# Kernel optimization log

Measured on AMD Instinct MI355X. Metric: run time of the kernel, lower is better.

The kernel has to match this reference:

```python
import jax, jax.numpy as jnp
import numpy as np

N_NODES = 50000
N_EDGES = 800000
D_IN = 128
H1 = 128
H2 = 64
N_CLASSES = 4


def _sage_conv(x, src, dst, w_l, w_r, b, num_nodes):
    # PyG SAGEConv (aggr='mean'): out = lin_l(mean_{j->i} x_j) + lin_r(x_i)
    ones = jnp.ones((src.shape[0],), dtype=x.dtype)
    deg = jax.ops.segment_sum(ones, dst, num_segments=num_nodes)  # [N]
    agg = jax.ops.segment_sum(x[src], dst, num_segments=num_nodes)  # [N, d]
    agg = agg / jnp.maximum(deg, 1.0)[:, None]
    return agg @ w_l + b + x @ w_r


def setup_inputs() -> dict:
    key = jax.random.key(0)
    ks = jax.random.split(key, 12)
    x_content = jax.random.normal(ks[0], (N_NODES, D_IN), dtype=jnp.float32)
    edge_index = jax.random.randint(ks[1], (2, N_EDGES), 0, N_NODES, dtype=jnp.int32)
    edge_type = jax.random.randint(ks[2], (N_EDGES,), 0, 4, dtype=jnp.int32)
    s = 0.05
    params = {
        'w_l0': jax.random.normal(ks[3], (D_IN, H1), jnp.float32) * s,
        'w_r0': jax.random.normal(ks[4], (D_IN, H1), jnp.float32) * s,
        'b0': jnp.zeros((H1,), jnp.float32),
        'w_l1': jax.random.normal(ks[5], (H1, H1), jnp.float32) * s,
        'w_r1': jax.random.normal(ks[6], (H1, H1), jnp.float32) * s,
        'b1': jnp.zeros((H1,), jnp.float32),
        'w_l2': jax.random.normal(ks[7], (H1, H2), jnp.float32) * s,
        'w_r2': jax.random.normal(ks[8], (H1, H2), jnp.float32) * s,
        'b2': jnp.zeros((H2,), jnp.float32),
        'w_out': jax.random.normal(ks[9], (H2, N_CLASSES), jnp.float32) * s,
        'b_out': jnp.zeros((N_CLASSES,), jnp.float32),
    }
    return {'x_content': x_content, 'edge_index': edge_index, 'edge_type': edge_type, **params}


def reference(x_content, edge_index, edge_type,
              w_l0, w_r0, b0, w_l1, w_r1, b1, w_l2, w_r2, b2, w_out, b_out):
    # eval mode: dropout is identity
    src, dst = edge_index[0], edge_index[1]
    n = x_content.shape[0]
    x = x_content
    for (wl, wr, b) in ((w_l0, w_r0, b0), (w_l1, w_r1, b1), (w_l2, w_r2, b2)):
        x = _sage_conv(x, src, dst, wl, wr, b, n)
        x = jax.nn.relu(x)
    return x @ w_out + b_out
```

## Files before the change

kernel.cpp:

```cpp
#include <hip/hip_runtime.h>
#include <hip/hip_fp16.h>

#define D 128

constexpr int RSH = 14;
constexpr int RSZ = 1 << RSH;
constexpr int NRANGE = 4;
constexpr int CSH = 15;
constexpr int CSZ = 1 << CSH;

using short8 = __attribute__((ext_vector_type(8))) short;
using f32x4 = __attribute__((ext_vector_type(4))) float;

__device__ inline void splitf(float v, unsigned short& h, unsigned short& l) {
    unsigned b = __float_as_uint(v);
    h = (unsigned short)(b >> 16);
    float fh = __uint_as_float(b & 0xffff0000u);
    float r = v - fh;
    l = (unsigned short)(__float_as_uint(r) >> 16);
}

struct WSplitArgs {
    const float* src[6];
    unsigned short* dh[6];
    unsigned short* dl[6];
    int n[6];
};

__global__ __launch_bounds__(256) void split_w(WSplitArgs a) {
    int m = blockIdx.y;
    int N = a.n[m];
    int e = blockIdx.x * 256 + threadIdx.x;
    if (e >= 128 * N) return;
    int sh = (N == 128) ? 7 : 6;
    int k = e >> sh;
    int n = e & (N - 1);
    float v = a.src[m][e];
    unsigned short h, l;
    splitf(v, h, l);
    a.dh[m][n * 128 + k] = h;
    a.dl[m][n * 128 + k] = l;
}

__global__ __launch_bounds__(1024) void hist_gemm_x(
    const int* __restrict__ dst, unsigned* __restrict__ hist,
    unsigned short* __restrict__ rank, int n_edges, int nchunk, int nhist,
    const float* __restrict__ X,
    const unsigned short* __restrict__ W1h, const unsigned short* __restrict__ W1l,
    const unsigned short* __restrict__ W2h, const unsigned short* __restrict__ W2l,
    const float* __restrict__ bias, __half* __restrict__ P, float* __restrict__ Q, int M) {
    __shared__ __align__(16) char smem[2 * 16 * 65 * 16];

    const int b = blockIdx.x;
    const int tid = threadIdx.x;

    if (b < nhist) {
        unsigned* lh = (unsigned*)smem;
        int r = b & (NRANGE - 1), c = b >> 2;
        for (int i = tid; i < RSZ / 2; i += 1024) lh[i] = 0;
        __syncthreads();
        int e0 = c << CSH, e1 = min(n_edges, e0 + CSZ);
        for (int e = e0 + tid; e < e1; e += 1024) {
            int d = dst[e];
            if ((d >> RSH) == r) {
                int ii = d & (RSZ - 1);
                unsigned sh = (ii & 1) * 16;
                unsigned old = atomicAdd(&lh[ii >> 1], 1u << sh);
                rank[e] = (unsigned short)((old >> sh) & 0xffffu);
            }
        }
        __syncthreads();
        unsigned* gh = hist + (size_t)(r * nchunk + c) * (RSZ / 2);
        for (int i = tid; i < RSZ / 2; i += 1024) gh[i] = lh[i];
        return;
    }

    short8(*As)[16 * 65] = (short8(*)[16 * 65])smem;
    const int wave = tid >> 6;
    const int lane = tid & 63;
    const int l15 = lane & 15;
    const int q = lane >> 4;
    const int m0 = (b - nhist) * 64;

    {
        int row = tid >> 4, col16 = tid & 15;
        int gr = min(m0 + row, M - 1);
        const float4* xp = (const float4*)X + (size_t)gr * 32 + col16 * 2;
        float4 v0 = xp[0], v1 = xp[1];
        float fv[8] = {v0.x, v0.y, v0.z, v0.w, v1.x, v1.y, v1.z, v1.w};
        short8 h, l;
#pragma unroll
        for (int j = 0; j < 8; ++j) {
            unsigned short hh_, ll_;
            splitf(fv[j], hh_, ll_);
            h[j] = (short)hh_;
            l[j] = (short)ll_;
        }
        As[0][col16 * 65 + row] = h;
        As[1][col16 * 65 + row] = l;
    }
    __syncthreads();

    const int isQ = wave >> 3;
    const int colbase = (wave & 7) * 16;
    const unsigned short* Wh = isQ ? W2h : W1h;
    const unsigned short* Wl = isQ ? W2l : W1l;
    const float bv = isQ ? bias[colbase + l15] : 0.f;

    f32x4 acc[4] = {};

#pragma unroll 1
    for (int kt = 0; kt < 4; ++kt) {
        int c = colbase + l15;
        int woff = c * 128 + kt * 32 + q * 8;
        short8 Bh = *(const short8*)(Wh + woff);
        short8 Bl = *(const short8*)(Wl + woff);
#pragma unroll
        for (int mt = 0; mt < 4; ++mt) {
            int ai = (kt * 4 + q) * 65 + mt * 16 + l15;
            short8 Afh = As[0][ai];
            short8 Afl = As[1][ai];
            acc[mt] = __builtin_amdgcn_mfma_f32_16x16x32_bf16(Afh, Bh, acc[mt], 0, 0, 0);
            acc[mt] = __builtin_amdgcn_mfma_f32_16x16x32_bf16(Afh, Bl, acc[mt], 0, 0, 0);
            acc[mt] = __builtin_amdgcn_mfma_f32_16x16x32_bf16(Afl, Bh, acc[mt], 0, 0, 0);
        }
    }

    const int col = colbase + l15;
#pragma unroll
    for (int mt = 0; mt < 4; ++mt) {
        int orow = m0 + mt * 16 + q * 4;
#pragma unroll
        for (int r = 0; r < 4; ++r) {
            int rr = orow + r;
            if (rr < M) {
                if (isQ) Q[(size_t)rr * 128 + col] = acc[mt][r] + bv;
                else P[(size_t)rr * 128 + col] = __float2half(acc[mt][r]);
            }
        }
    }
}

__global__ __launch_bounds__(256) void deg_sum_partials(
    const unsigned short* __restrict__ hist16, int* __restrict__ deg,
    int* __restrict__ partials, int n_nodes, int nchunk) {
    __shared__ int sd[256];
    int b = blockIdx.x, t = threadIdx.x;
    int i = b * 256 + t;
    int s = 0;
    if (i < n_nodes) {
        int r = i >> RSH, ii = i & (RSZ - 1);
        const unsigned short* hp = hist16 + (size_t)r * nchunk * RSZ + ii;
        for (int c = 0; c < nchunk; ++c) s += hp[(size_t)c * RSZ];
        deg[i] = s;
    }
    sd[t] = s;
    __syncthreads();
    for (int st = 128; st > 0; st >>= 1) {
        if (t < st) sd[t] += sd[t + st];
        __syncthreads();
    }
    if (t == 0) partials[b] = sd[0];
}

__global__ __launch_bounds__(256) void scan_fill(
    const int* __restrict__ deg, const int* __restrict__ partials,
    const unsigned short* __restrict__ hist16, int* __restrict__ row_ptr,
    float* __restrict__ inv_deg, int* __restrict__ base,
    int n_nodes, int nchunk, int nblk) {
    __shared__ int sp[256];
    __shared__ int sd[256];
    int b = blockIdx.x, t = threadIdx.x;

    sp[t] = (t < b && t < nblk) ? partials[t] : 0;
    __syncthreads();
    for (int st = 128; st > 0; st >>= 1) {
        if (t < st) sp[t] += sp[t + st];
        __syncthreads();
    }
    int pbase = sp[0];

    int i = b * 256 + t;
    int v = (i < n_nodes) ? deg[i] : 0;
    sd[t] = v;
    __syncthreads();
    for (int d = 1; d < 256; d <<= 1) {
        int x = (t >= d) ? sd[t - d] : 0;
        __syncthreads();
        sd[t] += x;
        __syncthreads();
    }
    int excl = sd[t] - v + pbase;
    if (i < n_nodes) {
        row_ptr[i] = excl;
        int dv = v > 1 ? v : 1;
        inv_deg[i] = 1.0f / (float)dv;
        if (i == n_nodes - 1) row_ptr[n_nodes] = excl + v;
        int r = i >> RSH, ii = i & (RSZ - 1);
        int bacc = excl;
        for (int c = 0; c < nchunk; ++c) {
            size_t idx = (size_t)(r * nchunk + c) * RSZ + ii;
            base[idx] = bacc;
            bacc += hist16[idx];
        }
    }
}

__global__ __launch_bounds__(256) void fill_edges(
    const int* __restrict__ src, const int* __restrict__ dst,
    const unsigned short* __restrict__ rank, const int* __restrict__ base,
    int* __restrict__ csr, int n_edges, int nchunk) {
    int e = blockIdx.x * 256 + threadIdx.x;
    if (e >= n_edges) return;
    int d = dst[e];
    int c = e >> CSH;
    int r = d >> RSH;
    int slot = base[(size_t)(r * nchunk + c) * RSZ + (d & (RSZ - 1))] + rank[e];
    csr[slot] = src[e];
}

template <int BN, int NT>
__global__ __launch_bounds__(256) void gemm_lds(
    const unsigned short* __restrict__ Ah, const unsigned short* __restrict__ Al,
    const unsigned short* __restrict__ W1h, const unsigned short* __restrict__ W1l,
    const unsigned short* __restrict__ W2h, const unsigned short* __restrict__ W2l,
    const float* __restrict__ bias, __half* __restrict__ P, float* __restrict__ Q, int M) {
    __shared__ short8 As[2][16 * 65];

    const int tid = threadIdx.x;
    const int wave = tid >> 6;
    const int lane = tid & 63;
    const int l15 = lane & 15;
    const int q = lane >> 4;
    const int m0 = blockIdx.x * 64;

#pragma unroll
    for (int it = 0; it < 8; ++it) {
        int s = it * 256 + tid;
        int arr = s >> 10;
        int sp = s & 1023;
        int row = sp >> 4, col16 = sp & 15;
        int gr = min(m0 + row, M - 1);
        const unsigned short* src = (arr ? Al : Ah) + (size_t)gr * 128 + col16 * 8;
        As[arr][col16 * 65 + row] = *(const short8*)src;
    }
    __syncthreads();

    const int isQ = wave >> 1;
    const int colbase = (wave & 1) * (NT * 16);
    const unsigned short* Wh = isQ ? W2h : W1h;
    const unsigned short* Wl = isQ ? W2l : W1l;

    float bvs[NT];
#pragma unroll
    for (int nt = 0; nt < NT; ++nt) bvs[nt] = isQ ? bias[colbase + nt * 16 + l15] : 0.f;

    f32x4 acc[4][NT] = {};

#pragma unroll 1
    for (int kt = 0; kt < 4; ++kt) {
        short8 Bh[NT], Bl[NT];
#pragma unroll
        for (int nt = 0; nt < NT; ++nt) {
            int c = colbase + nt * 16 + l15;
            int off = c * 128 + kt * 32 + q * 8;
            Bh[nt] = *(const short8*)(Wh + off);
            Bl[nt] = *(const short8*)(Wl + off);
        }
#pragma unroll
        for (int mt = 0; mt < 4; ++mt) {
            int ai = (kt * 4 + q) * 65 + mt * 16 + l15;
            short8 Afh = As[0][ai];
            short8 Afl = As[1][ai];
#pragma unroll
            for (int nt = 0; nt < NT; ++nt) {
                acc[mt][nt] = __builtin_amdgcn_mfma_f32_16x16x32_bf16(Afh, Bh[nt], acc[mt][nt], 0, 0, 0);
                acc[mt][nt] = __builtin_amdgcn_mfma_f32_16x16x32_bf16(Afh, Bl[nt], acc[mt][nt], 0, 0, 0);
                acc[mt][nt] = __builtin_amdgcn_mfma_f32_16x16x32_bf16(Afl, Bh[nt], acc[mt][nt], 0, 0, 0);
            }
        }
    }

#pragma unroll
    for (int mt = 0; mt < 4; ++mt) {
        int orow = m0 + mt * 16 + q * 4;
#pragma unroll
        for (int nt = 0; nt < NT; ++nt) {
            int col = colbase + nt * 16 + l15;
#pragma unroll
            for (int r = 0; r < 4; ++r) {
                int rr = orow + r;
                if (rr < M) {
                    if (isQ) Q[(size_t)rr * BN + col] = acc[mt][nt][r] + bvs[nt];
                    else P[(size_t)rr * BN + col] = __float2half(acc[mt][nt][r]);
                }
            }
        }
    }
}

__global__ __launch_bounds__(256) void agg_fused128(
    const __half* __restrict__ P, const float* __restrict__ Q,
    const int* __restrict__ row_ptr, const int* __restrict__ csr,
    const float* __restrict__ inv_deg, unsigned short* __restrict__ Hh,
    unsigned short* __restrict__ Hl, int n_nodes) {
    int node = (blockIdx.x * blockDim.x + threadIdx.x) >> 6;
    int lane = threadIdx.x & 63;
    if (node >= n_nodes) return;
    int beg = row_ptr[node], end = row_ptr[node + 1];
    const int g = lane >> 4;
    const int l = lane & 15;
    float a[4][8] = {};
    int e = beg;
    bool have = (e + 16 <= end);
    int i0 = 0, i1 = 0, i2 = 0, i3 = 0;
    if (have) { i0 = csr[e + g]; i1 = csr[e + 4 + g]; i2 = csr[e + 8 + g]; i3 = csr[e + 12 + g]; }
    while (have) {
        int en = e + 16;
        bool hn = (en + 16 <= end);
        int n0 = 0, n1 = 0, n2 = 0, n3 = 0;
        if (hn) { n0 = csr[en + g]; n1 = csr[en + 4 + g]; n2 = csr[en + 8 + g]; n3 = csr[en + 12 + g]; }
        int ss[4] = {i0, i1, i2, i3};
#pragma unroll
        for (int j = 0; j < 4; ++j) {
            uint4 raw = *(const uint4*)(P + (size_t)ss[j] * 128 + l * 8);
            float2 f01 = __half22float2(*reinterpret_cast<__half2*>(&raw.x));
            float2 f23 = __half22float2(*reinterpret_cast<__half2*>(&raw.y));
            float2 f45 = __half22float2(*reinterpret_cast<__half2*>(&raw.z));
            float2 f67 = __half22float2(*reinterpret_cast<__half2*>(&raw.w));
            a[j][0] += f01.x; a[j][1] += f01.y; a[j][2] += f23.x; a[j][3] += f23.y;
            a[j][4] += f45.x; a[j][5] += f45.y; a[j][6] += f67.x; a[j][7] += f67.y;
        }
        e = en; i0 = n0; i1 = n1; i2 = n2; i3 = n3; have = hn;
    }
    if (e < end) {
        int p0 = e + g, p1 = e + 4 + g, p2 = e + 8 + g, p3 = e + 12 + g;
        int j0 = (p0 < end) ? csr[p0] : -1;
        int j1 = (p1 < end) ? csr[p1] : -1;
        int j2 = (p2 < end) ? csr[p2] : -1;
        int j3 = (p3 < end) ? csr[p3] : -1;
        int ss[4] = {j0, j1, j2, j3};
#pragma unroll
        for (int j = 0; j < 4; ++j) {
            if (ss[j] >= 0) {
                uint4 raw = *(const uint4*)(P + (size_t)ss[j] * 128 + l * 8);
                float2 f01 = __half22float2(*reinterpret_cast<__half2*>(&raw.x));
                float2 f23 = __half22float2(*reinterpret_cast<__half2*>(&raw.y));
                float2 f45 = __half22float2(*reinterpret_cast<__half2*>(&raw.z));
                float2 f67 = __half22float2(*reinterpret_cast<__half2*>(&raw.w));
                a[j][0] += f01.x; a[j][1] += f01.y; a[j][2] += f23.x; a[j][3] += f23.y;
                a[j][4] += f45.x; a[j][5] += f45.y; a[j][6] += f67.x; a[j][7] += f67.y;
            }
        }
    }
    float s[8];
#pragma unroll
    for (int k = 0; k < 8; ++k) {
        s[k] = (a[0][k] + a[1][k]) + (a[2][k] + a[3][k]);
        s[k] += __shfl_xor(s[k], 16);
        s[k] += __shfl_xor(s[k], 32);
    }
    if (lane < 16) {
        float w = inv_deg[node];
        const float4* Q4 = (const float4*)Q;
        float4 q0 = Q4[(size_t)node * 32 + 2 * l];
        float4 q1 = Q4[(size_t)node * 32 + 2 * l + 1];
        float h0 = fmaxf(fmaf(s[0], w, q0.x), 0.f);
        float h1 = fmaxf(fmaf(s[1], w, q0.y), 0.f);
        float h2 = fmaxf(fmaf(s[2], w, q0.z), 0.f);
        float h3 = fmaxf(fmaf(s[3], w, q0.w), 0.f);
        float h4 = fmaxf(fmaf(s[4], w, q1.x), 0.f);
        float h5 = fmaxf(fmaf(s[5], w, q1.y), 0.f);
        float h6 = fmaxf(fmaf(s[6], w, q1.z), 0.f);
        float h7 = fmaxf(fmaf(s[7], w, q1.w), 0.f);
        ushort4 hv0, lv0, hv1, lv1;
        splitf(h0, hv0.x, lv0.x);
        splitf(h1, hv0.y, lv0.y);
        splitf(h2, hv0.z, lv0.z);
        splitf(h3, hv0.w, lv0.w);
        splitf(h4, hv1.x, lv1.x);
        splitf(h5, hv1.y, lv1.y);
        splitf(h6, hv1.z, lv1.z);
        splitf(h7, hv1.w, lv1.w);
        ((ushort4*)Hh)[(size_t)node * 32 + 2 * l] = hv0;
        ((ushort4*)Hh)[(size_t)node * 32 + 2 * l + 1] = hv1;
        ((ushort4*)Hl)[(size_t)node * 32 + 2 * l] = lv0;
        ((ushort4*)Hl)[(size_t)node * 32 + 2 * l + 1] = lv1;
    }
}

__global__ __launch_bounds__(256) void agg64_head(
    const __half* __restrict__ P, const float* __restrict__ Q,
    const int* __restrict__ row_ptr, const int* __restrict__ csr,
    const float* __restrict__ inv_deg, const float* __restrict__ Wo,
    const float* __restrict__ bo, float* __restrict__ out, int n_nodes) {
    int node = (blockIdx.x * blockDim.x + threadIdx.x) >> 6;
    int lane = threadIdx.x & 63;
    if (node >= n_nodes) return;
    int beg = row_ptr[node], end = row_ptr[node + 1];
    const int g = lane >> 4;
    const int l = lane & 15;
    float a[4][4] = {};
    int e = beg;
    bool have = (e + 16 <= end);
    int i0 = 0, i1 = 0, i2 = 0, i3 = 0;
    if (have) { i0 = csr[e + g]; i1 = csr[e + 4 + g]; i2 = csr[e + 8 + g]; i3 = csr[e + 12 + g]; }
    while (have) {
        int en = e + 16;
        bool hn = (en + 16 <= end);
        int n0 = 0, n1 = 0, n2 = 0, n3 = 0;
        if (hn) { n0 = csr[en + g]; n1 = csr[en + 4 + g]; n2 = csr[en + 8 + g]; n3 = csr[en + 12 + g]; }
        int ss[4] = {i0, i1, i2, i3};
#pragma unroll
        for (int j = 0; j < 4; ++j) {
            uint2 raw = *(const uint2*)(P + (size_t)ss[j] * 64 + l * 4);
            float2 f01 = __half22float2(*reinterpret_cast<__half2*>(&raw.x));
            float2 f23 = __half22float2(*reinterpret_cast<__half2*>(&raw.y));
            a[j][0] += f01.x; a[j][1] += f01.y; a[j][2] += f23.x; a[j][3] += f23.y;
        }
        e = en; i0 = n0; i1 = n1; i2 = n2; i3 = n3; have = hn;
    }
    if (e < end) {
        int p0 = e + g, p1 = e + 4 + g, p2 = e + 8 + g, p3 = e + 12 + g;
        int j0 = (p0 < end) ? csr[p0] : -1;
        int j1 = (p1 < end) ? csr[p1] : -1;
        int j2 = (p2 < end) ? csr[p2] : -1;
        int j3 = (p3 < end) ? csr[p3] : -1;
        int ss[4] = {j0, j1, j2, j3};
#pragma unroll
        for (int j = 0; j < 4; ++j) {
            if (ss[j] >= 0) {
                uint2 raw = *(const uint2*)(P + (size_t)ss[j] * 64 + l * 4);
                float2 f01 = __half22float2(*reinterpret_cast<__half2*>(&raw.x));
                float2 f23 = __half22float2(*reinterpret_cast<__half2*>(&raw.y));
                a[j][0] += f01.x; a[j][1] += f01.y; a[j][2] += f23.x; a[j][3] += f23.y;
            }
        }
    }
    float s0 = (a[0][0] + a[1][0]) + (a[2][0] + a[3][0]);
    float s1 = (a[0][1] + a[1][1]) + (a[2][1] + a[3][1]);
    float s2 = (a[0][2] + a[1][2]) + (a[2][2] + a[3][2]);
    float s3 = (a[0][3] + a[1][3]) + (a[2][3] + a[3][3]);
    s0 += __shfl_xor(s0, 16); s0 += __shfl_xor(s0, 32);
    s1 += __shfl_xor(s1, 16); s1 += __shfl_xor(s1, 32);
    s2 += __shfl_xor(s2, 16); s2 += __shfl_xor(s2, 32);
    s3 += __shfl_xor(s3, 16); s3 += __shfl_xor(s3, 32);
    if (lane < 16) {
        float w = inv_deg[node];
        float4 qv = ((const float4*)Q)[(size_t)node * 16 + l];
        float h0 = fmaxf(fmaf(s0, w, qv.x), 0.f);
        float h1 = fmaxf(fmaf(s1, w, qv.y), 0.f);
        float h2 = fmaxf(fmaf(s2, w, qv.z), 0.f);
        float h3 = fmaxf(fmaf(s3, w, qv.w), 0.f);
        const float4* Wo4 = (const float4*)Wo;
        float4 w0 = Wo4[4 * l + 0], w1 = Wo4[4 * l + 1], w2 = Wo4[4 * l + 2], w3 = Wo4[4 * l + 3];
        float c0 = h0 * w0.x + h1 * w1.x + h2 * w2.x + h3 * w3.x;
        float c1 = h0 * w0.y + h1 * w1.y + h2 * w2.y + h3 * w3.y;
        float c2 = h0 * w0.z + h1 * w1.z + h2 * w2.z + h3 * w3.z;
        float c3 = h0 * w0.w + h1 * w1.w + h2 * w2.w + h3 * w3.w;
#pragma unroll
        for (int m = 8; m > 0; m >>= 1) {
            c0 += __shfl_xor(c0, m);
            c1 += __shfl_xor(c1, m);
            c2 += __shfl_xor(c2, m);
            c3 += __shfl_xor(c3, m);
        }
        if (l == 0) {
            float4 r;
            r.x = c0 + bo[0];
            r.y = c1 + bo[1];
            r.z = c2 + bo[2];
            r.w = c3 + bo[3];
            ((float4*)out)[node] = r;
        }
    }
}

extern "C" void kernel_launch(void* const* d_in, const int* in_sizes, int n_in,
                              void* d_out, int out_size, void* d_ws, size_t ws_size,
                              hipStream_t stream) {
    const float* x = (const float*)d_in[0];
    const int* ei = (const int*)d_in[1];
    const float* wl0 = (const float*)d_in[3];
    const float* wr0 = (const float*)d_in[4];
    const float* b0 = (const float*)d_in[5];
    const float* wl1 = (const float*)d_in[6];
    const float* wr1 = (const float*)d_in[7];
    const float* b1 = (const float*)d_in[8];
    const float* wl2 = (const float*)d_in[9];
    const float* wr2 = (const float*)d_in[10];
    const float* b2 = (const float*)d_in[11];
    const float* wo = (const float*)d_in[12];
    const float* bo = (const float*)d_in[13];

    const int n_nodes = in_sizes[0] / D;
    const int n_edges = in_sizes[1] / 2;
    const int* srcp = ei;
    const int* dstp = ei + n_edges;

    char* ws = (char*)d_ws;
    size_t off = 0;
    auto carve = [&](size_t bytes) -> void* {
        void* p = ws + off;
        off = (off + bytes + 255) & ~(size_t)255;
        return p;
    };
    int* deg = (int*)carve((size_t)n_nodes * 4);
    int* row_ptr = (int*)carve((size_t)(n_nodes + 1) * 4);
    int* partials = (int*)carve(256 * 4);
    float* inv_deg = (float*)carve((size_t)n_nodes * 4);
    unsigned short* rankb = (unsigned short*)carve((size_t)n_edges * 2);
    int* csr = (int*)carve((size_t)n_edges * 4);
    __half* Pbuf = (__half*)carve((size_t)n_nodes * D * 2);
    float* Qbuf = (float*)carve((size_t)n_nodes * D * 4);
    unsigned short* hh = (unsigned short*)carve((size_t)n_nodes * D * 2);
    unsigned short* hl = (unsigned short*)carve((size_t)n_nodes * D * 2);
    unsigned short* wt = (unsigned short*)carve((size_t)(4 * 128 * 128 + 2 * 64 * 128) * 2 * 2);
    unsigned short* wl0h = wt;
    unsigned short* wl0l = wl0h + 128 * 128;
    unsigned short* wr0h = wl0l + 128 * 128;
    unsigned short* wr0l = wr0h + 128 * 128;
    unsigned short* wl1h = wr0l + 128 * 128;
    unsigned short* wl1l = wl1h + 128 * 128;
    unsigned short* wr1h = wl1l + 128 * 128;
    unsigned short* wr1l = wr1h + 128 * 128;
    unsigned short* wl2h = wr1l + 128 * 128;
    unsigned short* wl2l = wl2h + 64 * 128;
    unsigned short* wr2h = wl2l + 64 * 128;
    unsigned short* wr2l = wr2h + 64 * 128;

    const int nchunk = (n_edges + CSZ - 1) >> CSH;
    unsigned* hist = (unsigned*)carve((size_t)NRANGE * nchunk * (RSZ / 2) * 4);
    unsigned short* hist16 = (unsigned short*)hist;
    int* basep = (int*)carve((size_t)NRANGE * nchunk * RSZ * 4);

    const int nblk = (n_nodes + 255) / 256;
    const int nhist = NRANGE * nchunk;
    const int gemm_blocks = (n_nodes + 63) / 64;
    const int agg_blocks = (n_nodes * 64 + 255) / 256;

    WSplitArgs wa;
    wa.src[0] = wl0; wa.dh[0] = wl0h; wa.dl[0] = wl0l; wa.n[0] = 128;
    wa.src[1] = wr0; wa.dh[1] = wr0h; wa.dl[1] = wr0l; wa.n[1] = 128;
    wa.src[2] = wl1; wa.dh[2] = wl1h; wa.dl[2] = wl1l; wa.n[2] = 128;
    wa.src[3] = wr1; wa.dh[3] = wr1h; wa.dl[3] = wr1l; wa.n[3] = 128;
    wa.src[4] = wl2; wa.dh[4] = wl2h; wa.dl[4] = wl2l; wa.n[4] = 64;
    wa.src[5] = wr2; wa.dh[5] = wr2h; wa.dl[5] = wr2l; wa.n[5] = 64;

    split_w<<<dim3(64, 6), 256, 0, stream>>>(wa);
    hist_gemm_x<<<nhist + gemm_blocks, 1024, 0, stream>>>(
        dstp, hist, rankb, n_edges, nchunk, nhist,
        x, wl0h, wl0l, wr0h, wr0l, b0, Pbuf, Qbuf, n_nodes);
    deg_sum_partials<<<nblk, 256, 0, stream>>>(hist16, deg, partials, n_nodes, nchunk);
    scan_fill<<<nblk, 256, 0, stream>>>(deg, partials, hist16, row_ptr, inv_deg, basep,
                                        n_nodes, nchunk, nblk);
    fill_edges<<<(n_edges + 255) / 256, 256, 0, stream>>>(srcp, dstp, rankb, basep, csr,
                                                          n_edges, nchunk);
    agg_fused128<<<agg_blocks, 256, 0, stream>>>(Pbuf, Qbuf, row_ptr, csr, inv_deg, hh, hl, n_nodes);
    gemm_lds<128, 4><<<gemm_blocks, 256, 0, stream>>>(
        hh, hl, wl1h, wl1l, wr1h, wr1l, b1, Pbuf, Qbuf, n_nodes);
    agg_fused128<<<agg_blocks, 256, 0, stream>>>(Pbuf, Qbuf, row_ptr, csr, inv_deg, hh, hl, n_nodes);
    gemm_lds<64, 2><<<gemm_blocks, 256, 0, stream>>>(
        hh, hl, wl2h, wl2l, wr2h, wr2l, b2, Pbuf, Qbuf, n_nodes);
    agg64_head<<<agg_blocks, 256, 0, stream>>>(Pbuf, Qbuf, row_ptr, csr, inv_deg,
                                               wo, bo, (float*)d_out, n_nodes);
}
```

Measured before the change: 295.0 us.

## Widen layer GEMMs to one 16-column tile per wave and prefetch weights

Replaces the 4-wave gemm_lds kernel with gemm_wide, which launches one wave per 16-column output tile (1024 threads for 128 columns, 512 for 64), so each wave holds a single accumulator set instead of NT of them. Both this kernel and the fused first-layer GEMM now load the next k-step's weight fragments before issuing the current step's MFMAs. The aim is more waves in flight to hide latency, lower register pressure, and overlapping global weight loads with compute. In exchange, the larger blocks may limit how many blocks fit per CU, and each wave now re-reads the shared A tile from LDS on its own.

```diff
diff --git a/kernel.cpp b/kernel.cpp
--- a/kernel.cpp
+++ b/kernel.cpp
@@ -106,15 +106,19 @@
     const unsigned short* Wh = isQ ? W2h : W1h;
     const unsigned short* Wl = isQ ? W2l : W1l;
     const float bv = isQ ? bias[colbase + l15] : 0.f;
+    const int wbase = (colbase + l15) * 128 + q * 8;
 
     f32x4 acc[4] = {};
+    short8 Bh = *(const short8*)(Wh + wbase);
+    short8 Bl = *(const short8*)(Wl + wbase);
 
 #pragma unroll 1
     for (int kt = 0; kt < 4; ++kt) {
-        int c = colbase + l15;
-        int woff = c * 128 + kt * 32 + q * 8;
-        short8 Bh = *(const short8*)(Wh + woff);
-        short8 Bl = *(const short8*)(Wl + woff);
+        short8 nBh, nBl;
+        if (kt < 3) {
+            nBh = *(const short8*)(Wh + wbase + (kt + 1) * 32);
+            nBl = *(const short8*)(Wl + wbase + (kt + 1) * 32);
+        }
 #pragma unroll
         for (int mt = 0; mt < 4; ++mt) {
             int ai = (kt * 4 + q) * 65 + mt * 16 + l15;
@@ -124,6 +128,7 @@
             acc[mt] = __builtin_amdgcn_mfma_f32_16x16x32_bf16(Afh, Bl, acc[mt], 0, 0, 0);
             acc[mt] = __builtin_amdgcn_mfma_f32_16x16x32_bf16(Afl, Bh, acc[mt], 0, 0, 0);
         }
+        Bh = nBh; Bl = nBl;
     }
 
     const int col = colbase + l15;
@@ -219,13 +224,15 @@
     csr[slot] = src[e];
 }
 
-template <int BN, int NT>
-__global__ __launch_bounds__(256) void gemm_lds(
+template <int BN>
+__global__ __launch_bounds__(2 * (BN / 16) * 64) void gemm_wide(
     const unsigned short* __restrict__ Ah, const unsigned short* __restrict__ Al,
     const unsigned short* __restrict__ W1h, const unsigned short* __restrict__ W1l,
     const unsigned short* __restrict__ W2h, const unsigned short* __restrict__ W2l,
     const float* __restrict__ bias, __half* __restrict__ P, float* __restrict__ Q, int M) {
     __shared__ short8 As[2][16 * 65];
+    constexpr int NW = BN / 16;
+    constexpr int NTH = 2 * NW * 64;
 
     const int tid = threadIdx.x;
     const int wave = tid >> 6;
@@ -235,8 +242,8 @@
     const int m0 = blockIdx.x * 64;
 
 #pragma unroll
-    for (int it = 0; it < 8; ++it) {
-        int s = it * 256 + tid;
+    for (int it = 0; it < 2048 / NTH; ++it) {
+        int s = it * NTH + tid;
         int arr = s >> 10;
         int sp = s & 1023;
         int row = sp >> 4, col16 = sp & 15;
@@ -246,54 +253,46 @@
     }
     __syncthreads();
 
-    const int isQ = wave >> 1;
-    const int colbase = (wave & 1) * (NT * 16);
+    const int isQ = wave >= NW;
+    const int colbase = (isQ ? (wave - NW) : wave) * 16;
     const unsigned short* Wh = isQ ? W2h : W1h;
     const unsigned short* Wl = isQ ? W2l : W1l;
-
-    float bvs[NT];
-#pragma unroll
-    for (int nt = 0; nt < NT; ++nt) bvs[nt] = isQ ? bias[colbase + nt * 16 + l15] : 0.f;
-
-    f32x4 acc[4][NT] = {};
+    const float bv = isQ ? bias[colbase + l15] : 0.f;
+    const int wbase = (colbase + l15) * 128 + q * 8;
+
+    f32x4 acc[4] = {};
+    short8 Bh = *(const short8*)(Wh + wbase);
+    short8 Bl = *(const short8*)(Wl + wbase);
 
 #pragma unroll 1
     for (int kt = 0; kt < 4; ++kt) {
-        short8 Bh[NT], Bl[NT];
-#pragma unroll
-        for (int nt = 0; nt < NT; ++nt) {
-            int c = colbase + nt * 16 + l15;
-            int off = c * 128 + kt * 32 + q * 8;
-            Bh[nt] = *(const short8*)(Wh + off);
-            Bl[nt] = *(const short8*)(Wl + off);
+        short8 nBh, nBl;
+        if (kt < 3) {
+            nBh = *(const short8*)(Wh + wbase + (kt + 1) * 32);
+            nBl = *(const short8*)(Wl + wbase + (kt + 1) * 32);
         }
 #pragma unroll
         for (int mt = 0; mt < 4; ++mt) {
             int ai = (kt * 4 + q) * 65 + mt * 16 + l15;
             short8 Afh = As[0][ai];
             short8 Afl = As[1][ai];
-#pragma unroll
-            for (int nt = 0; nt < NT; ++nt) {
-                acc[mt][nt] = __builtin_amdgcn_mfma_f32_16x16x32_bf16(Afh, Bh[nt], acc[mt][nt], 0, 0, 0);
-                acc[mt][nt] = __builtin_amdgcn_mfma_f32_16x16x32_bf16(Afh, Bl[nt], acc[mt][nt], 0, 0, 0);
-                acc[mt][nt] = __builtin_amdgcn_mfma_f32_16x16x32_bf16(Afl, Bh[nt], acc[mt][nt], 0, 0, 0);
-            }
-        }
-    }
-
+            acc[mt] = __builtin_amdgcn_mfma_f32_16x16x32_bf16(Afh, Bh, acc[mt], 0, 0, 0);
+            acc[mt] = __builtin_amdgcn_mfma_f32_16x16x32_bf16(Afh, Bl, acc[mt], 0, 0, 0);
+            acc[mt] = __builtin_amdgcn_mfma_f32_16x16x32_bf16(Afl, Bh, acc[mt], 0, 0, 0);
+        }
+        Bh = nBh; Bl = nBl;
+    }
+
+    const int col = colbase + l15;
 #pragma unroll
     for (int mt = 0; mt < 4; ++mt) {
         int orow = m0 + mt * 16 + q * 4;
 #pragma unroll
-        for (int nt = 0; nt < NT; ++nt) {
-            int col = colbase + nt * 16 + l15;
-#pragma unroll
-            for (int r = 0; r < 4; ++r) {
-                int rr = orow + r;
-                if (rr < M) {
-                    if (isQ) Q[(size_t)rr * BN + col] = acc[mt][nt][r] + bvs[nt];
-                    else P[(size_t)rr * BN + col] = __float2half(acc[mt][nt][r]);
-                }
+        for (int r = 0; r < 4; ++r) {
+            int rr = orow + r;
+            if (rr < M) {
+                if (isQ) Q[(size_t)rr * BN + col] = acc[mt][r] + bv;
+                else P[(size_t)rr * BN + col] = __float2half(acc[mt][r]);
             }
         }
     }
@@ -557,10 +556,10 @@
     fill_edges<<<(n_edges + 255) / 256, 256, 0, stream>>>(srcp, dstp, rankb, basep, csr,
                                                           n_edges, nchunk);
     agg_fused128<<<agg_blocks, 256, 0, stream>>>(Pbuf, Qbuf, row_ptr, csr, inv_deg, hh, hl, n_nodes);
-    gemm_lds<128, 4><<<gemm_blocks, 256, 0, stream>>>(
+    gemm_wide<128><<<gemm_blocks, 1024, 0, stream>>>(
         hh, hl, wl1h, wl1l, wr1h, wr1l, b1, Pbuf, Qbuf, n_nodes);
     agg_fused128<<<agg_blocks, 256, 0, stream>>>(Pbuf, Qbuf, row_ptr, csr, inv_deg, hh, hl, n_nodes);
-    gemm_lds<64, 2><<<gemm_blocks, 256, 0, stream>>>(
+    gemm_wide<64><<<gemm_blocks, 512, 0, stream>>>(
         hh, hl, wl2h, wl2l, wr2h, wr2l, b2, Pbuf, Qbuf, n_nodes);
     agg64_head<<<agg_blocks, 256, 0, stream>>>(Pbuf, Qbuf, row_ptr, csr, inv_deg,
                                                wo, bo, (float*)d_out, n_nodes);
```

Result: no change. 293.9 us (-0.4%).
